# Optimization experiments

Hardware: AMD Instinct MI355X
Metric: run time of the kernel (lower is better)

## Reference

```python
import jax, jax.numpy as jnp
import numpy as np

BS, S, WIDTH, MODES = 2, 512, 64, 16
P = S * (S - 1) // 2
IU, JU = np.triu_indices(S, 1)  # upper-triangle (i<j) index constants
COLL_COEF = 0.9  # training=True path


def spectral_conv(x, w):
    # x: (bs, c_in, n), w: (c_in, c_out, modes, 2)
    n = x.shape[-1]
    xf = jnp.fft.rfft(x, axis=2, norm='ortho')  # (bs, c_in, n//2+1) complex
    wm = w[..., 0] + 1j * w[..., 1]
    out_m = jnp.einsum('bix,iox->box', xf[:, :, :MODES], wm)
    pad = jnp.zeros((x.shape[0], w.shape[1], n // 2 + 1 - MODES), dtype=out_m.dtype)
    return jnp.fft.irfft(jnp.concatenate([out_m, pad], axis=2), n=n, axis=2, norm='ortho')


def dsmc(x, a, rvec):
    # x, a: (bs, c, n); rvec: (bs, c, P) unit vectors along c.  dt=1, v = a*dt.
    bs, c, n = x.shape
    v = a
    x_r = jnp.linalg.norm(x[:, :, :, None] - x[:, :, None, :], axis=1)  # (bs, n, n)
    v_r = jnp.linalg.norm(v[:, :, :, None] - v[:, :, None, :], axis=1)
    v_cm = (v[:, :, :, None] + v[:, :, None, :]) * 0.5  # (bs, c, n, n)
    x_cm = (x[:, :, :, None] + x[:, :, None, :]) * 0.5
    u_x = jnp.exp(-x_r)
    v_r_max = jnp.max(v_r, axis=(1, 2), keepdims=True)  # (bs,1,1)
    mask = v_r / v_r_max * u_x
    cm = mask > (1.0 - COLL_COEF)  # collision mask (bs, n, n)
    # antisymmetric projection of v_r upper triangle onto random unit vectors
    proj = v_r[:, IU, JU][:, None, :] * rvec  # (bs, c, P)
    vrl = (jnp.zeros((bs, c, n, n), x.dtype)
           .at[:, :, IU, JU].set(proj)
           .at[:, :, JU, IU].set(-proj))
    delta_v = v_cm + vrl - v[:, :, :, None]
    cmf = cm.astype(x.dtype)
    v_new = v + jnp.sum(delta_v * cmf[:, None], axis=2)  # sum over partners i
    cmf = cmf + jnp.eye(n, dtype=x.dtype)[None]  # add self
    x_new = jnp.sum(x_cm * cmf[:, None], axis=2) / jnp.sum(cmf, axis=2)[:, None, :]
    x_new = x_new + v_new  # x = x + v*dt
    return x_new, v_new


def setup_inputs() -> dict:
    key = jax.random.key(0)
    ks = jax.random.split(key, 12)
    x = jax.random.normal(ks[0], (BS, S, 2), jnp.float32)
    v = jax.random.normal(ks[1], (BS, WIDTH, S), jnp.float32)
    vecs = jax.random.normal(ks[2], (4, BS, WIDTH, P), jnp.float32)
    vecs = vecs / jnp.linalg.norm(vecs, axis=2, keepdims=True)  # unit vectors over chnl
    fc0_w = jax.random.normal(ks[3], (2, WIDTH), jnp.float32) * 0.5
    fc0_b = jax.random.normal(ks[4], (WIDTH,), jnp.float32) * 0.1
    scale = 1.0 / (WIDTH * WIDTH)
    spec_w = jax.random.uniform(ks[5], (4, WIDTH, WIDTH, MODES, 2), jnp.float32) * scale
    conv_w = jax.random.normal(ks[6], (4, WIDTH, WIDTH), jnp.float32) * (WIDTH ** -0.5)
    conv_b = jax.random.normal(ks[7], (4, WIDTH), jnp.float32) * 0.05
    fc1_w = jax.random.normal(ks[8], (WIDTH, 128), jnp.float32) * (WIDTH ** -0.5)
    fc1_b = jnp.zeros((128,), jnp.float32)
    fc2_w = jax.random.normal(ks[9], (128, 1), jnp.float32) * (128 ** -0.5)
    fc2_b = jnp.zeros((1,), jnp.float32)
    return {"x": x, "v": v, "vecs": vecs, "fc0_w": fc0_w, "fc0_b": fc0_b,
            "spec_w": spec_w, "conv_w": conv_w, "conv_b": conv_b,
            "fc1_w": fc1_w, "fc1_b": fc1_b, "fc2_w": fc2_w, "fc2_b": fc2_b}


def reference(x, v, vecs, fc0_w, fc0_b, spec_w, conv_w, conv_b, fc1_w, fc1_b, fc2_w, fc2_b):
    # NOTE: v is overwritten by a*dt inside KINET_DSMC2 in the original; kept for signature fidelity.
    h = x @ fc0_w + fc0_b          # (bs, s, width)
    h = jnp.transpose(h, (0, 2, 1))  # (bs, width, s)
    for i in range(4):
        a = spectral_conv(h, spec_w[i])
        p = jnp.einsum('oi,bin->bon', conv_w[i], h) + conv_b[i][None, :, None]
        h, vv = dsmc(p, a, vecs[i])
        if i < 3:
            h = jax.nn.relu(h)
    h = jnp.transpose(h, (0, 2, 1))  # (bs, s, width)
    h = jax.nn.relu(h @ fc1_w + fc1_b)
    return h @ fc2_w + fc2_b  # (bs, s, 1)
```

## Files before the change

kernel.cpp:

```cpp
#include <hip/hip_runtime.h>
#include <math.h>

#define S 512
#define W 64
#define MODES 16
#define PAIRS 130816
#define INV_SQRT_N 0.04419417382415922f
#define TWO_PI_OVER_N 0.012271846303085130f

__global__ __launch_bounds__(256) void k_fc0(const float* __restrict__ x,
                                             const float* __restrict__ w,
                                             const float* __restrict__ bias,
                                             float* __restrict__ h) {
    int b = blockIdx.x >> 6, c = blockIdx.x & 63;
    int tid = threadIdx.x;
    float w0 = w[c], w1 = w[64 + c], bb = bias[c];
    for (int t = tid; t < S; t += 256) {
        float x0 = x[(b * S + t) * 2];
        float x1 = x[(b * S + t) * 2 + 1];
        h[(b * W + c) * S + t] = x0 * w0 + x1 * w1 + bb;
    }
}

__global__ __launch_bounds__(256) void k_fft(const float* __restrict__ h,
                                             float* __restrict__ Xf) {
    int b = blockIdx.x >> 6, ch = blockIdx.x & 63;
    int tid = threadIdx.x;
    const float* hp = h + (b * W + ch) * S;
    float v0 = hp[tid], v1 = hp[tid + 256];
    float re[MODES], im[MODES];
#pragma unroll
    for (int m = 0; m < MODES; ++m) {
        float sn, cs;
        sincosf(TWO_PI_OVER_N * (float)(m * tid), &sn, &cs);
        float a = (m & 1) ? (v0 - v1) : (v0 + v1);
        re[m] = a * cs;
        im[m] = -a * sn;
    }
    __shared__ float part[4][32];
    int lane = tid & 63, wv = tid >> 6;
#pragma unroll
    for (int m = 0; m < MODES; ++m) {
        float r = re[m], ii = im[m];
        for (int off = 32; off; off >>= 1) {
            r += __shfl_down(r, off);
            ii += __shfl_down(ii, off);
        }
        if (lane == 0) { part[wv][2 * m] = r; part[wv][2 * m + 1] = ii; }
    }
    __syncthreads();
    if (tid < 32) {
        float s = part[0][tid] + part[1][tid] + part[2][tid] + part[3][tid];
        Xf[(b * W + ch) * 32 + tid] = s * INV_SQRT_N;
    }
}

__global__ __launch_bounds__(256) void k_mix(const float* __restrict__ Xf,
                                             const float* __restrict__ specw,
                                             float* __restrict__ Y, int l) {
    int b = blockIdx.x >> 6, o = blockIdx.x & 63;
    int tid = threadIdx.x, m = tid & 15, ip = tid >> 4;
    __shared__ float Xs[2048];
    for (int idx = tid; idx < 2048; idx += 256) Xs[idx] = Xf[b * 2048 + idx];
    __syncthreads();
    float ar = 0.f, ai = 0.f;
#pragma unroll
    for (int q = 0; q < 4; ++q) {
        int i = ip * 4 + q;
        const float* wp = specw + (size_t)(((l * W + i) * W + o) * MODES + m) * 2;
        float wr = wp[0], wi = wp[1];
        float xr = Xs[i * 32 + 2 * m], xi = Xs[i * 32 + 2 * m + 1];
        ar += xr * wr - xi * wi;
        ai += xr * wi + xi * wr;
    }
    __shared__ float redr[16][17], redi[16][17];
    redr[ip][m] = ar; redi[ip][m] = ai;
    __syncthreads();
    if (tid < 16) {
        float sr = 0.f, si = 0.f;
        for (int p = 0; p < 16; ++p) { sr += redr[p][tid]; si += redi[p][tid]; }
        Y[(b * W + o) * 32 + 2 * tid] = sr;
        Y[(b * W + o) * 32 + 2 * tid + 1] = si;
    }
}

__global__ __launch_bounds__(256) void k_irfft(const float* __restrict__ Y,
                                               float* __restrict__ aT) {
    int blk = blockIdx.x;
    int b = blk >> 4, t0 = (blk & 15) * 32;
    int tid = threadIdx.x;
    int o = tid & 63, tg = tid >> 6;
    __shared__ float Ys[2048];
    for (int idx = tid; idx < 2048; idx += 256) Ys[idx] = Y[b * 2048 + idx];
    __syncthreads();
    float yr[MODES], yi[MODES];
#pragma unroll
    for (int m = 0; m < MODES; ++m) {
        yr[m] = Ys[o * 32 + 2 * m];
        yi[m] = Ys[o * 32 + 2 * m + 1];
    }
    float cc[MODES], ss[MODES], cd[MODES], sd[MODES];
#pragma unroll
    for (int m = 1; m < MODES; ++m) {
        sincosf(TWO_PI_OVER_N * (float)(m * (t0 + tg)), &ss[m], &cc[m]);
        sincosf(TWO_PI_OVER_N * (float)(4 * m), &sd[m], &cd[m]);
    }
    for (int tt = 0; tt < 8; ++tt) {
        int t = t0 + tg + 4 * tt;
        float acc = yr[0];
#pragma unroll
        for (int m = 1; m < MODES; ++m) {
            acc += 2.0f * (yr[m] * cc[m] - yi[m] * ss[m]);
            float nc = cc[m] * cd[m] - ss[m] * sd[m];
            float ns = ss[m] * cd[m] + cc[m] * sd[m];
            cc[m] = nc; ss[m] = ns;
        }
        aT[(b * S + t) * W + o] = acc * INV_SQRT_N;
    }
}

__global__ __launch_bounds__(256) void k_conv(const float* __restrict__ h,
                                              const float* __restrict__ convw,
                                              const float* __restrict__ convb,
                                              float* __restrict__ pT,
                                              unsigned* __restrict__ vmax, int l) {
    int blk = blockIdx.x;
    int b = blk >> 4, t0 = (blk & 15) * 32;
    int tid = threadIdx.x;
    int o = tid & 63, tg = tid >> 6;
    if (blk == 0 && tid < 2) vmax[tid] = 0u;
    __shared__ float hs[64 * 33];
    __shared__ float wsh[64 * 65];
    for (int idx = tid; idx < 2048; idx += 256) {
        int r = idx >> 5, t = idx & 31;
        hs[r * 33 + t] = h[(b * W + r) * S + t0 + t];
    }
    for (int idx = tid; idx < 4096; idx += 256) {
        wsh[(idx >> 6) * 65 + (idx & 63)] = convw[l * 4096 + idx];
    }
    __syncthreads();
    float wreg[64];
#pragma unroll
    for (int i = 0; i < W; ++i) wreg[i] = wsh[o * 65 + i];
    float bias = convb[l * W + o];
    for (int tt = 0; tt < 8; ++tt) {
        int tl = tg * 8 + tt;
        float acc = bias;
#pragma unroll
        for (int i = 0; i < W; ++i) acc = fmaf(wreg[i], hs[i * 33 + tl], acc);
        pT[(b * S + t0 + tl) * W + o] = acc;
    }
}

__global__ __launch_bounds__(256) void k_pair(const float* __restrict__ pT,
                                              const float* __restrict__ aT,
                                              float* __restrict__ vr,
                                              float* __restrict__ uxm,
                                              unsigned* __restrict__ vmax) {
    int blk = blockIdx.x;
    int b = blk >> 8;
    int rest = blk & 255;
    int i0 = (rest & 15) * 32, j0 = (rest >> 4) * 32;
    int tid = threadIdx.x;
    int tx = tid & 15, ty = tid >> 4;
    __shared__ float Pi[64 * 33], Pj[64 * 33], Vi[64 * 33], Vj[64 * 33];
    for (int idx = tid; idx < 2048; idx += 256) {
        int k = idx >> 6, c = idx & 63;
        Pi[c * 33 + k] = pT[(b * S + i0 + k) * W + c];
        Pj[c * 33 + k] = pT[(b * S + j0 + k) * W + c];
        Vi[c * 33 + k] = aT[(b * S + i0 + k) * W + c];
        Vj[c * 33 + k] = aT[(b * S + j0 + k) * W + c];
    }
    __syncthreads();
    float ax[2][2] = {{0.f, 0.f}, {0.f, 0.f}};
    float av[2][2] = {{0.f, 0.f}, {0.f, 0.f}};
    for (int c = 0; c < W; ++c) {
        float pi0 = Pi[c * 33 + 2 * tx], pi1 = Pi[c * 33 + 2 * tx + 1];
        float pj0 = Pj[c * 33 + 2 * ty], pj1 = Pj[c * 33 + 2 * ty + 1];
        float vi0 = Vi[c * 33 + 2 * tx], vi1 = Vi[c * 33 + 2 * tx + 1];
        float vj0 = Vj[c * 33 + 2 * ty], vj1 = Vj[c * 33 + 2 * ty + 1];
        float d;
        d = pi0 - pj0; ax[0][0] = fmaf(d, d, ax[0][0]);
        d = pi1 - pj0; ax[1][0] = fmaf(d, d, ax[1][0]);
        d = pi0 - pj1; ax[0][1] = fmaf(d, d, ax[0][1]);
        d = pi1 - pj1; ax[1][1] = fmaf(d, d, ax[1][1]);
        d = vi0 - vj0; av[0][0] = fmaf(d, d, av[0][0]);
        d = vi1 - vj0; av[1][0] = fmaf(d, d, av[1][0]);
        d = vi0 - vj1; av[0][1] = fmaf(d, d, av[0][1]);
        d = vi1 - vj1; av[1][1] = fmaf(d, d, av[1][1]);
    }
    float mx = 0.f;
#pragma unroll
    for (int jj = 0; jj < 2; ++jj) {
#pragma unroll
        for (int ii = 0; ii < 2; ++ii) {
            int i = i0 + 2 * tx + ii, j = j0 + 2 * ty + jj;
            float xr = sqrtf(ax[ii][jj]);
            float vv = sqrtf(av[ii][jj]);
            vr[((size_t)b * S + j) * S + i] = vv;
            uxm[((size_t)b * S + j) * S + i] = expf(-xr);
            mx = fmaxf(mx, vv);
        }
    }
    for (int off = 32; off; off >>= 1) mx = fmaxf(mx, __shfl_xor(mx, off));
    if ((tid & 63) == 0) atomicMax(&vmax[b], __float_as_uint(mx));
}

__global__ __launch_bounds__(256) void k_mask(const float* __restrict__ vr,
                                              const float* __restrict__ uxm,
                                              const unsigned* __restrict__ vmaxu,
                                              const float* __restrict__ aT,
                                              const float* __restrict__ pT,
                                              float* __restrict__ wpair,
                                              float* __restrict__ sv,
                                              float* __restrict__ sx,
                                              int* __restrict__ Acnt,
                                              float* __restrict__ Tg) {
    int b = blockIdx.x >> 9, j = blockIdx.x & 511;
    int tid = threadIdx.x, lane = tid & 63, wv = tid >> 6;
    __shared__ float wrow[S];
    __shared__ float SV[4][64], SX[4][64];
    __shared__ int cnt4[4];
    const float* vrp = vr + ((size_t)b * S + j) * S;
    const float* uxp = uxm + ((size_t)b * S + j) * S;
    float vmax = __uint_as_float(vmaxu[b]);
    int mycnt = 0;
    for (int i = tid; i < S; i += 256) {
        float v = vrp[i], u = uxp[i];
        bool act = (v / vmax) * u > 0.1f;
        wrow[i] = act ? v : 0.f;
        mycnt += act ? 1 : 0;
    }
    for (int o = 32; o; o >>= 1) mycnt += __shfl_down(mycnt, o);
    if (lane == 0) cnt4[wv] = mycnt;
    __syncthreads();
    int A = cnt4[0] + cnt4[1] + cnt4[2] + cnt4[3];
    if (tid == 0) Acnt[b * S + j] = A;
    if (tid < 64) Tg[((size_t)b * S + j) * W + tid] = 0.f;
    size_t tri = (size_t)j * 511 - (((size_t)j * (j - 1)) >> 1);
    for (int i = j + 1 + tid; i < S; i += 256)
        wpair[(size_t)b * PAIRS + tri + (i - j - 1)] = wrow[i];
    float svp = 0.f, sxp = 0.f;
    const float* aTb = aT + (size_t)b * S * W;
    const float* pTb = pT + (size_t)b * S * W;
    for (int k = 0; k < 128; ++k) {
        int i = wv * 128 + k;
        float w01 = (wrow[i] != 0.f) ? 1.0f : 0.0f;
        svp = fmaf(w01, aTb[i * W + lane], svp);
        sxp = fmaf(w01, pTb[i * W + lane], sxp);
    }
    SV[wv][lane] = svp; SX[wv][lane] = sxp;
    __syncthreads();
    if (tid < 64) {
        sv[((size_t)b * S + j) * W + tid] = SV[0][tid] + SV[1][tid] + SV[2][tid] + SV[3][tid];
        sx[((size_t)b * S + j) * W + tid] = SX[0][tid] + SX[1][tid] + SX[2][tid] + SX[3][tid];
    }
}

__global__ __launch_bounds__(256) void k_proj2(const float* __restrict__ wpair,
                                               const float* __restrict__ vecs,
                                               float* __restrict__ Tg, int l) {
    int tile = blockIdx.x, cg = blockIdx.y, b = blockIdx.z;
    int ti = 0, rem = tile;
    while (rem >= 8 - ti) { rem -= 8 - ti; ++ti; }
    int tj = ti + rem;
    int i0 = ti * 64, j0 = tj * 64;
    int tid = threadIdx.x, lane = tid & 63, wv = tid >> 6;
    __shared__ float Tjs[4][64][9];
    __shared__ float Tis[64][9];
    for (int k2 = tid; k2 < 4 * 64 * 9; k2 += 256) ((float*)Tjs)[k2] = 0.f;
    for (int k2 = tid; k2 < 64 * 9; k2 += 256) ((float*)Tis)[k2] = 0.f;
    __syncthreads();
    const float* wb = wpair + (size_t)b * PAIRS;
    const float* Rb = vecs + (size_t)((l * 2 + b) * W + cg * 8) * PAIRS;
    float accj[8] = {0.f, 0.f, 0.f, 0.f, 0.f, 0.f, 0.f, 0.f};
    int gj = j0 + lane;
    for (int s = 0; s < 16; ++s) {
        int li = wv + 4 * s;
        int gi = i0 + li;
        int pbase = gi * 511 - ((gi * (gi - 1)) >> 1) + (j0 - gi - 1);
        bool valid = gj > gi;
        int idx = valid ? (pbase + lane) : 0;
        float w = wb[idx];
        if (!valid) w = 0.f;
        if (__ballot(w != 0.f) == 0ull) continue;
        float part[8];
#pragma unroll
        for (int cc = 0; cc < 8; ++cc) {
            float r = Rb[(size_t)cc * PAIRS + idx];
            float p = w * r;
            accj[cc] += p;
            part[cc] = p;
        }
#pragma unroll
        for (int cc = 0; cc < 8; ++cc) {
            float p = part[cc];
            for (int o = 32; o; o >>= 1) p += __shfl_xor(p, o);
            if (lane == 0) Tis[li][cc] = p;
        }
    }
#pragma unroll
    for (int cc = 0; cc < 8; ++cc) Tjs[wv][lane][cc] = accj[cc];
    __syncthreads();
    for (int k2 = tid; k2 < 512; k2 += 256) {
        int r = k2 >> 3, cc = k2 & 7;
        float sj = Tjs[0][r][cc] + Tjs[1][r][cc] + Tjs[2][r][cc] + Tjs[3][r][cc];
        if (sj != 0.f)
            atomicAdd(&Tg[((size_t)b * S + j0 + r) * W + cg * 8 + cc], sj);
        float si = Tis[r][cc];
        if (si != 0.f)
            atomicAdd(&Tg[((size_t)b * S + i0 + r) * W + cg * 8 + cc], -si);
    }
}

__global__ __launch_bounds__(256) void k_fin(const float* __restrict__ aT,
                                             const float* __restrict__ pT,
                                             const float* __restrict__ sv,
                                             const float* __restrict__ sx,
                                             const int* __restrict__ Acnt,
                                             const float* __restrict__ Tg,
                                             float* __restrict__ h_std,
                                             float* __restrict__ hT,
                                             int do_relu) {
    int g = blockIdx.x * 4 + (threadIdx.x >> 6);
    int b = g >> 9, j = g & 511;
    int c = threadIdx.x & 63;
    size_t row = ((size_t)b * S + j) * W;
    float A = (float)Acnt[b * S + j];
    float vj = aT[row + c], xj = pT[row + c];
    float vnew = vj + 0.5f * (A * vj - sv[row + c]) + Tg[row + c];
    float accx = 0.5f * (A * xj + sx[row + c]);
    float xnew = (xj + accx) / (A + 1.0f) + vnew;
    if (do_relu) xnew = fmaxf(xnew, 0.0f);
    hT[row + c] = xnew;
    h_std[((size_t)b * W + c) * S + j] = xnew;
}

__global__ __launch_bounds__(128) void k_head(const float* __restrict__ hT,
                                              const float* __restrict__ fc1w,
                                              const float* __restrict__ fc1b,
                                              const float* __restrict__ fc2w,
                                              const float* __restrict__ fc2b,
                                              float* __restrict__ out) {
    int blk = blockIdx.x;
    int b = blk >> 9, t = blk & 511;
    int k = threadIdx.x;
    __shared__ float hsh[64];
    __shared__ float red[2];
    if (k < 64) hsh[k] = hT[(b * S + t) * W + k];
    __syncthreads();
    float acc = fc1b[k];
#pragma unroll
    for (int c = 0; c < W; ++c) acc = fmaf(hsh[c], fc1w[c * 128 + k], acc);
    acc = fmaxf(acc, 0.f);
    float p = acc * fc2w[k];
    for (int off = 32; off; off >>= 1) p += __shfl_down(p, off);
    int lane = k & 63, wv = k >> 6;
    if (lane == 0) red[wv] = p;
    __syncthreads();
    if (k == 0) out[b * S + t] = red[0] + red[1] + fc2b[0];
}

extern "C" void kernel_launch(void* const* d_in, const int* in_sizes, int n_in,
                              void* d_out, int out_size, void* d_ws, size_t ws_size,
                              hipStream_t stream) {
    const float* x = (const float*)d_in[0];
    const float* vecs = (const float*)d_in[2];
    const float* fc0w = (const float*)d_in[3];
    const float* fc0b = (const float*)d_in[4];
    const float* specw = (const float*)d_in[5];
    const float* convw = (const float*)d_in[6];
    const float* convb = (const float*)d_in[7];
    const float* fc1w = (const float*)d_in[8];
    const float* fc1b = (const float*)d_in[9];
    const float* fc2w = (const float*)d_in[10];
    const float* fc2b = (const float*)d_in[11];
    float* out = (float*)d_out;

    char* ws = (char*)d_ws;
    unsigned* vmax = (unsigned*)ws;
    float* h_std = (float*)(ws + 256);
    float* hT = h_std + 65536;
    float* aT = hT + 65536;
    float* pT = aT + 65536;
    float* Xf = pT + 65536;
    float* Yb = Xf + 4096;
    float* vrbuf = Yb + 4096;
    float* uxbuf = vrbuf + 524288;
    float* Tg = uxbuf + 524288;
    float* svb = Tg + 65536;
    float* sxb = svb + 65536;
    int* Acnt = (int*)(sxb + 65536);
    float* wpair = (float*)(Acnt + 1024);

    k_fc0<<<128, 256, 0, stream>>>(x, fc0w, fc0b, h_std);
    for (int l = 0; l < 4; ++l) {
        k_fft<<<128, 256, 0, stream>>>(h_std, Xf);
        k_mix<<<128, 256, 0, stream>>>(Xf, specw, Yb, l);
        k_irfft<<<32, 256, 0, stream>>>(Yb, aT);
        k_conv<<<32, 256, 0, stream>>>(h_std, convw, convb, pT, vmax, l);
        k_pair<<<512, 256, 0, stream>>>(pT, aT, vrbuf, uxbuf, vmax);
        k_mask<<<1024, 256, 0, stream>>>(vrbuf, uxbuf, vmax, aT, pT,
                                         wpair, svb, sxb, Acnt, Tg);
        k_proj2<<<dim3(36, 8, 2), 256, 0, stream>>>(wpair, vecs, Tg, l);
        k_fin<<<256, 256, 0, stream>>>(aT, pT, svb, sxb, Acnt, Tg,
                                       h_std, hT, (l < 3) ? 1 : 0);
    }
    k_head<<<1024, 128, 0, stream>>>(hT, fc1w, fc1b, fc2w, fc2b, out);
}
```

Measured before the change: 769.1 us.

## Fuse irfft with pointwise conv and fold MLP head into final kernel

Merges the inverse-FFT and 1x1 conv kernels into one kernel launched on many more blocks (4 positions per block instead of 32), computing sincos directly instead of by recurrence. The fc1/fc2 head is fused into the last-layer finalize kernel, removing a launch and the hT round trip. In the mask kernel the masked accumulation now uses a branch instead of a multiply by 0/1. Costs are more sincos work per output and per-block rereads of conv weights from global memory.

```diff
diff --git a/kernel.cpp b/kernel.cpp
--- a/kernel.cpp
+++ b/kernel.cpp
@@ -84,72 +84,52 @@
     }
 }
 
-__global__ __launch_bounds__(256) void k_irfft(const float* __restrict__ Y,
-                                               float* __restrict__ aT) {
+__global__ __launch_bounds__(256) void k_ac(const float* __restrict__ Y,
+                                            const float* __restrict__ h,
+                                            const float* __restrict__ convw,
+                                            const float* __restrict__ convb,
+                                            float* __restrict__ aT,
+                                            float* __restrict__ pT,
+                                            unsigned* __restrict__ vmax, int l) {
     int blk = blockIdx.x;
-    int b = blk >> 4, t0 = (blk & 15) * 32;
-    int tid = threadIdx.x;
-    int o = tid & 63, tg = tid >> 6;
-    __shared__ float Ys[2048];
-    for (int idx = tid; idx < 2048; idx += 256) Ys[idx] = Y[b * 2048 + idx];
-    __syncthreads();
-    float yr[MODES], yi[MODES];
-#pragma unroll
-    for (int m = 0; m < MODES; ++m) {
-        yr[m] = Ys[o * 32 + 2 * m];
-        yi[m] = Ys[o * 32 + 2 * m + 1];
-    }
-    float cc[MODES], ss[MODES], cd[MODES], sd[MODES];
-#pragma unroll
-    for (int m = 1; m < MODES; ++m) {
-        sincosf(TWO_PI_OVER_N * (float)(m * (t0 + tg)), &ss[m], &cc[m]);
-        sincosf(TWO_PI_OVER_N * (float)(4 * m), &sd[m], &cd[m]);
-    }
-    for (int tt = 0; tt < 8; ++tt) {
-        int t = t0 + tg + 4 * tt;
-        float acc = yr[0];
-#pragma unroll
-        for (int m = 1; m < MODES; ++m) {
-            acc += 2.0f * (yr[m] * cc[m] - yi[m] * ss[m]);
-            float nc = cc[m] * cd[m] - ss[m] * sd[m];
-            float ns = ss[m] * cd[m] + cc[m] * sd[m];
-            cc[m] = nc; ss[m] = ns;
-        }
-        aT[(b * S + t) * W + o] = acc * INV_SQRT_N;
-    }
-}
-
-__global__ __launch_bounds__(256) void k_conv(const float* __restrict__ h,
-                                              const float* __restrict__ convw,
-                                              const float* __restrict__ convb,
-                                              float* __restrict__ pT,
-                                              unsigned* __restrict__ vmax, int l) {
-    int blk = blockIdx.x;
-    int b = blk >> 4, t0 = (blk & 15) * 32;
+    int b = blk >> 7, t0 = (blk & 127) * 4;
     int tid = threadIdx.x;
     int o = tid & 63, tg = tid >> 6;
     if (blk == 0 && tid < 2) vmax[tid] = 0u;
-    __shared__ float hs[64 * 33];
-    __shared__ float wsh[64 * 65];
-    for (int idx = tid; idx < 2048; idx += 256) {
-        int r = idx >> 5, t = idx & 31;
-        hs[r * 33 + t] = h[(b * W + r) * S + t0 + t];
-    }
-    for (int idx = tid; idx < 4096; idx += 256) {
-        wsh[(idx >> 6) * 65 + (idx & 63)] = convw[l * 4096 + idx];
-    }
-    __syncthreads();
-    float wreg[64];
-#pragma unroll
-    for (int i = 0; i < W; ++i) wreg[i] = wsh[o * 65 + i];
-    float bias = convb[l * W + o];
-    for (int tt = 0; tt < 8; ++tt) {
-        int tl = tg * 8 + tt;
-        float acc = bias;
-#pragma unroll
-        for (int i = 0; i < W; ++i) acc = fmaf(wreg[i], hs[i * 33 + tl], acc);
-        pT[(b * S + t0 + tl) * W + o] = acc;
-    }
+    __shared__ float hs[64 * 5];
+    if (tid < 256) {
+        int r = tid >> 2, t = tid & 3;
+        hs[r * 5 + t] = h[(b * W + r) * S + t0 + t];
+    }
+    float yr[MODES], yi[MODES];
+    const float4* yp = (const float4*)(Y + b * 2048 + o * 32);
+#pragma unroll
+    for (int q = 0; q < 8; ++q) {
+        float4 y4 = yp[q];
+        yr[2 * q] = y4.x; yi[2 * q] = y4.y;
+        yr[2 * q + 1] = y4.z; yi[2 * q + 1] = y4.w;
+    }
+    int t = t0 + tg;
+    float acc = yr[0];
+#pragma unroll
+    for (int m = 1; m < MODES; ++m) {
+        float sn, cs;
+        sincosf(TWO_PI_OVER_N * (float)(m * t), &sn, &cs);
+        acc += 2.0f * (yr[m] * cs - yi[m] * sn);
+    }
+    aT[((size_t)b * S + t) * W + o] = acc * INV_SQRT_N;
+    __syncthreads();
+    float pacc = convb[l * W + o];
+    const float4* wp = (const float4*)(convw + l * 4096 + o * 64);
+#pragma unroll
+    for (int i4 = 0; i4 < 16; ++i4) {
+        float4 w4 = wp[i4];
+        pacc = fmaf(w4.x, hs[(4 * i4 + 0) * 5 + tg], pacc);
+        pacc = fmaf(w4.y, hs[(4 * i4 + 1) * 5 + tg], pacc);
+        pacc = fmaf(w4.z, hs[(4 * i4 + 2) * 5 + tg], pacc);
+        pacc = fmaf(w4.w, hs[(4 * i4 + 3) * 5 + tg], pacc);
+    }
+    pT[((size_t)b * S + t) * W + o] = pacc;
 }
 
 __global__ __launch_bounds__(256) void k_pair(const float* __restrict__ pT,
@@ -245,9 +225,10 @@
     const float* pTb = pT + (size_t)b * S * W;
     for (int k = 0; k < 128; ++k) {
         int i = wv * 128 + k;
-        float w01 = (wrow[i] != 0.f) ? 1.0f : 0.0f;
-        svp = fmaf(w01, aTb[i * W + lane], svp);
-        sxp = fmaf(w01, pTb[i * W + lane], sxp);
+        if (wrow[i] != 0.f) {
+            svp += aTb[i * W + lane];
+            sxp += pTb[i * W + lane];
+        }
     }
     SV[wv][lane] = svp; SX[wv][lane] = sxp;
     __syncthreads();
@@ -320,9 +301,14 @@
                                              const int* __restrict__ Acnt,
                                              const float* __restrict__ Tg,
                                              float* __restrict__ h_std,
-                                             float* __restrict__ hT,
-                                             int do_relu) {
-    int g = blockIdx.x * 4 + (threadIdx.x >> 6);
+                                             const float* __restrict__ fc1w,
+                                             const float* __restrict__ fc1b,
+                                             const float* __restrict__ fc2w,
+                                             const float* __restrict__ fc2b,
+                                             float* __restrict__ out,
+                                             int do_relu, int do_head) {
+    int wv = threadIdx.x >> 6;
+    int g = blockIdx.x * 4 + wv;
     int b = g >> 9, j = g & 511;
     int c = threadIdx.x & 63;
     size_t row = ((size_t)b * S + j) * W;
@@ -332,33 +318,23 @@
     float accx = 0.5f * (A * xj + sx[row + c]);
     float xnew = (xj + accx) / (A + 1.0f) + vnew;
     if (do_relu) xnew = fmaxf(xnew, 0.0f);
-    hT[row + c] = xnew;
-    h_std[((size_t)b * W + c) * S + j] = xnew;
-}
-
-__global__ __launch_bounds__(128) void k_head(const float* __restrict__ hT,
-                                              const float* __restrict__ fc1w,
-                                              const float* __restrict__ fc1b,
-                                              const float* __restrict__ fc2w,
-                                              const float* __restrict__ fc2b,
-                                              float* __restrict__ out) {
-    int blk = blockIdx.x;
-    int b = blk >> 9, t = blk & 511;
-    int k = threadIdx.x;
-    __shared__ float hsh[64];
-    __shared__ float red[2];
-    if (k < 64) hsh[k] = hT[(b * S + t) * W + k];
-    __syncthreads();
-    float acc = fc1b[k];
-#pragma unroll
-    for (int c = 0; c < W; ++c) acc = fmaf(hsh[c], fc1w[c * 128 + k], acc);
-    acc = fmaxf(acc, 0.f);
-    float p = acc * fc2w[k];
+    if (!do_head) {
+        h_std[((size_t)b * W + c) * S + j] = xnew;
+        return;
+    }
+    __shared__ float hsh[4][64];
+    hsh[wv][c] = xnew;
+    __syncthreads();
+    float a0 = fc1b[c], a1 = fc1b[c + 64];
+    for (int cc = 0; cc < W; ++cc) {
+        float hv = hsh[wv][cc];
+        a0 = fmaf(hv, fc1w[cc * 128 + c], a0);
+        a1 = fmaf(hv, fc1w[cc * 128 + c + 64], a1);
+    }
+    a0 = fmaxf(a0, 0.f); a1 = fmaxf(a1, 0.f);
+    float p = a0 * fc2w[c] + a1 * fc2w[c + 64];
     for (int off = 32; off; off >>= 1) p += __shfl_down(p, off);
-    int lane = k & 63, wv = k >> 6;
-    if (lane == 0) red[wv] = p;
-    __syncthreads();
-    if (k == 0) out[b * S + t] = red[0] + red[1] + fc2b[0];
+    if (c == 0) out[b * S + j] = p + fc2b[0];
 }
 
 extern "C" void kernel_launch(void* const* d_in, const int* in_sizes, int n_in,
@@ -392,19 +368,19 @@
     float* sxb = svb + 65536;
     int* Acnt = (int*)(sxb + 65536);
     float* wpair = (float*)(Acnt + 1024);
+    (void)hT;
 
     k_fc0<<<128, 256, 0, stream>>>(x, fc0w, fc0b, h_std);
     for (int l = 0; l < 4; ++l) {
         k_fft<<<128, 256, 0, stream>>>(h_std, Xf);
         k_mix<<<128, 256, 0, stream>>>(Xf, specw, Yb, l);
-        k_irfft<<<32, 256, 0, stream>>>(Yb, aT);
-        k_conv<<<32, 256, 0, stream>>>(h_std, convw, convb, pT, vmax, l);
+        k_ac<<<256, 256, 0, stream>>>(Yb, h_std, convw, convb, aT, pT, vmax, l);
         k_pair<<<512, 256, 0, stream>>>(pT, aT, vrbuf, uxbuf, vmax);
         k_mask<<<1024, 256, 0, stream>>>(vrbuf, uxbuf, vmax, aT, pT,
                                          wpair, svb, sxb, Acnt, Tg);
         k_proj2<<<dim3(36, 8, 2), 256, 0, stream>>>(wpair, vecs, Tg, l);
         k_fin<<<256, 256, 0, stream>>>(aT, pT, svb, sxb, Acnt, Tg,
-                                       h_std, hT, (l < 3) ? 1 : 0);
-    }
-    k_head<<<1024, 128, 0, stream>>>(hT, fc1w, fc1b, fc2w, fc2b, out);
-}
+                                       h_std, fc1w, fc1b, fc2w, fc2b, out,
+                                       (l < 3) ? 1 : 0, (l == 3) ? 1 : 0);
+    }
+}
```

Result: faster. 733.2 us (-4.7%).
